# Kernel tuning notes

Hardware: AMD Instinct MI355X
Metric: run time of the kernel (lower is better)

## Reference

```python
import jax, jax.numpy as jnp
import numpy as np


def _chamfer_sq(points, gts):
    # points: [B,N,3], gts: [B,M,3]
    pn = jnp.sum(points * points, axis=-1)              # [B,N]
    gn = jnp.sum(gts * gts, axis=-1)                    # [B,M]
    cross = jnp.einsum('bnd,bmd->bnm', points, gts)     # [B,N,M]
    d = pn[:, :, None] + gn[:, None, :] - 2.0 * cross   # [B,N,M]
    d = jnp.maximum(d, 0.0)
    p2g = jnp.min(d, axis=2)                            # [B,N] squared NN dist
    g2p = jnp.min(d, axis=1)                            # [B,M]
    return p2g, g2p


def setup_inputs() -> dict:
    key = jax.random.key(0)
    k1, k2 = jax.random.split(key)
    B, N, M = 8, 4096, 4096
    points = jax.random.normal(k1, (B, N, 3), dtype=jnp.float32)
    gts = jax.random.normal(k2, (B, M, 3), dtype=jnp.float32)
    return {"points": points, "gts": gts}


def reference(points, gts):
    p2g_sq, g2p_sq = _chamfer_sq(points, gts)
    p2g = jnp.sqrt(jnp.mean(p2g_sq, axis=1))   # [B]
    g2p = jnp.sqrt(jnp.mean(g2p_sq, axis=1))   # [B]
    loss = (p2g + g2p) / 2.0
    return (jnp.mean(loss), jnp.mean(p2g), jnp.mean(g2p))
```

## Files before the change

kernel.cpp:

```cpp
#include <hip/hip_runtime.h>
#include <math.h>

#define NPTS 4096
#define NB   8
#define QCB  512
#define RCB  1024
#define NQC  (NPTS / QCB)
#define NRC  (NPTS / RCB)

typedef _Float16 h8   __attribute__((ext_vector_type(8)));
typedef float    f32x16 __attribute__((ext_vector_type(16)));

__device__ __forceinline__ void split2(float v, _Float16& h, _Float16& l) {
    h = (_Float16)v;
    l = (_Float16)(v - (float)h);
}

__global__ __launch_bounds__(1024, 1) void chamfer_mfma32(
    const float* __restrict__ P, const float* __restrict__ G,
    float* __restrict__ qpart,
    float* __restrict__ rpart)
{
    __shared__ __align__(16) unsigned char smem[77824];
    h8*   Bfr  = (h8*)smem;
    int*  rbuf = (int*)(smem + 73728);
    float* qbufall = (float*)smem;

    const int b    = blockIdx.y;
    const int qc   = blockIdx.x >> 2;
    const int rc   = blockIdx.x & 3;
    const int tid  = threadIdx.x;
    const int w    = tid >> 6;
    const int lane = tid & 63;
    const int col  = lane & 31;
    const int kg   = lane >> 5;

    const float* __restrict__ Pb = P + (size_t)b * NPTS * 3;
    const float* __restrict__ Gb = G + (size_t)b * NPTS * 3;

    const _Float16 one = (_Float16)1.f, zr = (_Float16)0.f;

    rbuf[tid] = 0x7f7fffff;
    for (int e = tid; e < 32 * 64; e += 1024) {
        const int el   = e & 63;
        const int ecol = el & 31, ekg = el >> 5;
        const int ref  = rc * RCB + (e >> 6) * 32 + ecol;
        const float gx = Gb[3 * ref], gy = Gb[3 * ref + 1], gz = Gb[3 * ref + 2];
        const float gn = fmaf(gx, gx, fmaf(gy, gy, gz * gz));
        _Float16 xh, xl, yh, yl, zh, zl, nh, nl;
        split2(gx, xh, xl); split2(gy, yh, yl); split2(gz, zh, zl); split2(gn, nh, nl);
        Bfr[e] = ekg ? (h8){one, nh, xl, yl, zl, zr, nl, zr}
                     : (h8){xh, yh, zh, one, nh, xh, yh, zh};
    }

    {
    }
    const int q0 = qc * QCB + w * 32 + col;
    const float px = Pb[3 * q0], py = Pb[3 * q0 + 1], pz = Pb[3 * q0 + 2];
    const float m2x = -2.f * px, m2y = -2.f * py, m2z = -2.f * pz;
    const float pn = fmaf(px, px, fmaf(py, py, pz * pz));
    _Float16 axh, axl, ayh, ayl, azh, azl, aph, apl;
    split2(m2x, axh, axl); split2(m2y, ayh, ayl); split2(m2z, azh, azl); split2(pn, aph, apl);
    const h8 afr = kg ? (h8){apl, zr, axh, ayh, azh, aph, one, zr}
                      : (h8){axh, ayh, azh, aph, one, axl, ayl, azl};

    f32x16 qacc;
#pragma unroll
    for (int j = 0; j < 16; ++j) qacc[j] = 3.4e38f;

    __syncthreads();

    const f32x16 cz = (f32x16){0.f,0.f,0.f,0.f,0.f,0.f,0.f,0.f,
                               0.f,0.f,0.f,0.f,0.f,0.f,0.f,0.f};
#pragma unroll 4
    for (int rt = 0; rt < 32; ++rt) {
        const h8 bfr = Bfr[rt * 64 + lane];
        f32x16 d = __builtin_amdgcn_mfma_f32_32x32x16_f16(afr, bfr, cz, 0, 0, 0);
#pragma unroll
        for (int j = 0; j < 16; ++j) qacc[j] = fminf(qacc[j], d[j]);
        float t0 = fminf(fminf(d[0],  d[1]),  d[2]);
        float t1 = fminf(fminf(d[3],  d[4]),  d[5]);
        float t2 = fminf(fminf(d[6],  d[7]),  d[8]);
        float t3 = fminf(fminf(d[9],  d[10]), d[11]);
        float t4 = fminf(fminf(d[12], d[13]), d[14]);
        float v  = fminf(fminf(fminf(t0, t1), t2), fminf(fminf(t3, t4), d[15]));
        v = fmaxf(v, 0.f);
        atomicMin(&rbuf[rt * 32 + col], __float_as_int(v));
    }

    __syncthreads();
    rpart[((size_t)b * NQC + qc) * NPTS + rc * RCB + tid] = __int_as_float(rbuf[tid]);
    __syncthreads();

    float* qw = qbufall + w * 1152;
#pragma unroll
    for (int j = 0; j < 16; ++j) {
        const int row = (j & 3) + 8 * (j >> 2) + 4 * kg;
        qw[row * 36 + col] = qacc[j];
    }
    __syncthreads();
    const float4* qr = (const float4*)(qw + col * 36);
    float4 v0 = qr[0], v1 = qr[1], v2 = qr[2], v3 = qr[3];
    float4 v4 = qr[4], v5 = qr[5], v6 = qr[6], v7 = qr[7];
    float4 m01 = make_float4(fminf(v0.x,v1.x), fminf(v0.y,v1.y), fminf(v0.z,v1.z), fminf(v0.w,v1.w));
    float4 m23 = make_float4(fminf(v2.x,v3.x), fminf(v2.y,v3.y), fminf(v2.z,v3.z), fminf(v2.w,v3.w));
    float4 m45 = make_float4(fminf(v4.x,v5.x), fminf(v4.y,v5.y), fminf(v4.z,v5.z), fminf(v4.w,v5.w));
    float4 m67 = make_float4(fminf(v6.x,v7.x), fminf(v6.y,v7.y), fminf(v6.z,v7.z), fminf(v6.w,v7.w));
    float4 ma = make_float4(fminf(m01.x,m23.x), fminf(m01.y,m23.y), fminf(m01.z,m23.z), fminf(m01.w,m23.w));
    float4 mb = make_float4(fminf(m45.x,m67.x), fminf(m45.y,m67.y), fminf(m45.z,m67.z), fminf(m45.w,m67.w));
    const float rowmin = fminf(fminf(fminf(ma.x, ma.y), fminf(ma.z, ma.w)),
                               fminf(fminf(mb.x, mb.y), fminf(mb.z, mb.w)));
    if (lane < 32)
        qpart[((size_t)b * NRC + rc) * NPTS + qc * QCB + w * 32 + col] = rowmin;
}

__global__ __launch_bounds__(256) void chamfer_reduce2(
    const float* __restrict__ qpart, const float* __restrict__ rpart,
    float* __restrict__ r16)
{
    const int path = blockIdx.x >> 3;
    const int b    = blockIdx.x & 7;
    float sum = 0.f;
    if (path == 0) {
        const float* __restrict__ base = qpart + (size_t)b * NRC * NPTS;
        for (int i = 0; i < NPTS / 256; ++i) {
            const int qq = i * 256 + threadIdx.x;
            float mn = base[qq];
#pragma unroll
            for (int c = 1; c < NRC; ++c) mn = fminf(mn, base[(size_t)c * NPTS + qq]);
            sum += fmaxf(mn, 0.f);
        }
    } else {
        const float* __restrict__ base = rpart + (size_t)b * NQC * NPTS;
        for (int i = 0; i < NPTS / 256; ++i) {
            const int qq = i * 256 + threadIdx.x;
            float mn = base[qq];
#pragma unroll
            for (int c = 1; c < NQC; ++c) mn = fminf(mn, base[(size_t)c * NPTS + qq]);
            sum += fmaxf(mn, 0.f);
        }
    }
    __shared__ float red[256];
    red[threadIdx.x] = sum;
    __syncthreads();
    if (threadIdx.x < 128) red[threadIdx.x] += red[threadIdx.x + 128];
    __syncthreads();
    if (threadIdx.x < 64) {
        float v = red[threadIdx.x] + red[threadIdx.x + 64];
#pragma unroll
        for (int off = 32; off > 0; off >>= 1) v += __shfl_down(v, off, 64);
        if (threadIdx.x == 0) r16[blockIdx.x] = sqrtf(v / (float)NPTS);
    }
}

__global__ __launch_bounds__(64) void chamfer_final(
    const float* __restrict__ r16, float* __restrict__ out)
{
    if (threadIdx.x == 0) {
        float p2g = 0.f, g2p = 0.f;
#pragma unroll
        for (int bb = 0; bb < NB; ++bb) { p2g += r16[bb]; g2p += r16[NB + bb]; }
        p2g *= (1.0f / NB);
        g2p *= (1.0f / NB);
        out[0] = 0.5f * (p2g + g2p);
        out[1] = p2g;
        out[2] = g2p;
    }
}

extern "C" void kernel_launch(void* const* d_in, const int* in_sizes, int n_in,
                              void* d_out, int out_size, void* d_ws, size_t ws_size,
                              hipStream_t stream) {
    const float* points = (const float*)d_in[0];
    const float* gts    = (const float*)d_in[1];
    float* out = (float*)d_out;

    float* qpart = (float*)d_ws;
    float* rpart = qpart + (size_t)NB * NRC * NPTS;
    float* r16   = rpart + (size_t)NB * NQC * NPTS;

    dim3 grid1(NQC * NRC, NB);
    chamfer_mfma32<<<grid1, 1024, 0, stream>>>(points, gts, qpart, rpart);

    chamfer_reduce2<<<dim3(16), 256, 0, stream>>>(qpart, rpart, r16);

    chamfer_final<<<dim3(1), 64, 0, stream>>>(r16, out);
}
```

Before: 21.00 us.

## Halve reference chunk, allow two blocks per CU, fuse final reduction via last-block counter

The reference chunk per block drops from 1024 to 512, which doubles the grid to 512 blocks. Launch bounds now allow two 1024-thread blocks per CU, and LDS is reduced to fit. The reduce kernel is split into 64 blocks, and the last block to finish, found with an atomic counter, computes the final outputs, so the separate final kernel launch goes away. In exchange there are twice as many partial rows to reduce, plus atomic and threadfence overhead. Register pressure also rises under the two-block occupancy limit.

```diff
diff --git a/kernel.cpp b/kernel.cpp
--- a/kernel.cpp
+++ b/kernel.cpp
@@ -4,11 +4,12 @@
 #define NPTS 4096
 #define NB   8
 #define QCB  512
-#define RCB  1024
+#define RCB  512
 #define NQC  (NPTS / QCB)
 #define NRC  (NPTS / RCB)
+#define NRT  (RCB / 32)
 
-typedef _Float16 h8   __attribute__((ext_vector_type(8)));
+typedef _Float16 h8     __attribute__((ext_vector_type(8)));
 typedef float    f32x16 __attribute__((ext_vector_type(16)));
 
 __device__ __forceinline__ void split2(float v, _Float16& h, _Float16& l) {
@@ -16,32 +17,35 @@
     l = (_Float16)(v - (float)h);
 }
 
-__global__ __launch_bounds__(1024, 1) void chamfer_mfma32(
+__global__ __launch_bounds__(1024, 2) void chamfer_mfma32(
     const float* __restrict__ P, const float* __restrict__ G,
     float* __restrict__ qpart,
-    float* __restrict__ rpart)
+    float* __restrict__ rpart,
+    int* __restrict__ counter)
 {
-    __shared__ __align__(16) unsigned char smem[77824];
-    h8*   Bfr  = (h8*)smem;
-    int*  rbuf = (int*)(smem + 73728);
+    __shared__ __align__(16) unsigned char smem[73728];
+    h8*    Bfr  = (h8*)smem;
+    int*   rbuf = (int*)(smem + 16384);
     float* qbufall = (float*)smem;
 
     const int b    = blockIdx.y;
-    const int qc   = blockIdx.x >> 2;
-    const int rc   = blockIdx.x & 3;
+    const int qc   = blockIdx.x >> 3;
+    const int rc   = blockIdx.x & 7;
     const int tid  = threadIdx.x;
     const int w    = tid >> 6;
     const int lane = tid & 63;
     const int col  = lane & 31;
     const int kg   = lane >> 5;
 
+    if (blockIdx.x == 0 && blockIdx.y == 0 && tid == 0) *counter = 0;
+
     const float* __restrict__ Pb = P + (size_t)b * NPTS * 3;
     const float* __restrict__ Gb = G + (size_t)b * NPTS * 3;
 
     const _Float16 one = (_Float16)1.f, zr = (_Float16)0.f;
 
-    rbuf[tid] = 0x7f7fffff;
-    for (int e = tid; e < 32 * 64; e += 1024) {
+    if (tid < 512) rbuf[tid] = 0x7f7fffff;
+    for (int e = tid; e < NRT * 64; e += 1024) {
         const int el   = e & 63;
         const int ecol = el & 31, ekg = el >> 5;
         const int ref  = rc * RCB + (e >> 6) * 32 + ecol;
@@ -53,8 +57,6 @@
                      : (h8){xh, yh, zh, one, nh, xh, yh, zh};
     }
 
-    {
-    }
     const int q0 = qc * QCB + w * 32 + col;
     const float px = Pb[3 * q0], py = Pb[3 * q0 + 1], pz = Pb[3 * q0 + 2];
     const float m2x = -2.f * px, m2y = -2.f * py, m2z = -2.f * pz;
@@ -73,7 +75,7 @@
     const f32x16 cz = (f32x16){0.f,0.f,0.f,0.f,0.f,0.f,0.f,0.f,
                                0.f,0.f,0.f,0.f,0.f,0.f,0.f,0.f};
 #pragma unroll 4
-    for (int rt = 0; rt < 32; ++rt) {
+    for (int rt = 0; rt < NRT; ++rt) {
         const h8 bfr = Bfr[rt * 64 + lane];
         f32x16 d = __builtin_amdgcn_mfma_f32_32x32x16_f16(afr, bfr, cz, 0, 0, 0);
 #pragma unroll
@@ -89,7 +91,8 @@
     }
 
     __syncthreads();
-    rpart[((size_t)b * NQC + qc) * NPTS + rc * RCB + tid] = __int_as_float(rbuf[tid]);
+    if (tid < RCB)
+        rpart[((size_t)b * NQC + qc) * NPTS + rc * RCB + tid] = __int_as_float(rbuf[tid]);
     __syncthreads();
 
     float* qw = qbufall + w * 1152;
@@ -99,48 +102,42 @@
         qw[row * 36 + col] = qacc[j];
     }
     __syncthreads();
-    const float4* qr = (const float4*)(qw + col * 36);
-    float4 v0 = qr[0], v1 = qr[1], v2 = qr[2], v3 = qr[3];
-    float4 v4 = qr[4], v5 = qr[5], v6 = qr[6], v7 = qr[7];
-    float4 m01 = make_float4(fminf(v0.x,v1.x), fminf(v0.y,v1.y), fminf(v0.z,v1.z), fminf(v0.w,v1.w));
-    float4 m23 = make_float4(fminf(v2.x,v3.x), fminf(v2.y,v3.y), fminf(v2.z,v3.z), fminf(v2.w,v3.w));
-    float4 m45 = make_float4(fminf(v4.x,v5.x), fminf(v4.y,v5.y), fminf(v4.z,v5.z), fminf(v4.w,v5.w));
-    float4 m67 = make_float4(fminf(v6.x,v7.x), fminf(v6.y,v7.y), fminf(v6.z,v7.z), fminf(v6.w,v7.w));
-    float4 ma = make_float4(fminf(m01.x,m23.x), fminf(m01.y,m23.y), fminf(m01.z,m23.z), fminf(m01.w,m23.w));
-    float4 mb = make_float4(fminf(m45.x,m67.x), fminf(m45.y,m67.y), fminf(m45.z,m67.z), fminf(m45.w,m67.w));
-    const float rowmin = fminf(fminf(fminf(ma.x, ma.y), fminf(ma.z, ma.w)),
-                               fminf(fminf(mb.x, mb.y), fminf(mb.z, mb.w)));
-    if (lane < 32)
+    if (lane < 32) {
+        const float4* qr = (const float4*)(qw + col * 36);
+        float4 v = qr[0];
+#pragma unroll
+        for (int k = 1; k < 8; ++k) {
+            float4 u = qr[k];
+            v.x = fminf(v.x, u.x); v.y = fminf(v.y, u.y);
+            v.z = fminf(v.z, u.z); v.w = fminf(v.w, u.w);
+        }
+        const float rowmin = fminf(fminf(v.x, v.y), fminf(v.z, v.w));
         qpart[((size_t)b * NRC + rc) * NPTS + qc * QCB + w * 32 + col] = rowmin;
+    }
 }
 
 __global__ __launch_bounds__(256) void chamfer_reduce2(
     const float* __restrict__ qpart, const float* __restrict__ rpart,
-    float* __restrict__ r16)
+    float* __restrict__ sums, int* __restrict__ counter,
+    float* __restrict__ out)
 {
-    const int path = blockIdx.x >> 3;
-    const int b    = blockIdx.x & 7;
+    const int path = blockIdx.x >> 5;
+    const int b    = (blockIdx.x >> 2) & 7;
+    const int sp   = blockIdx.x & 3;
+    const float* __restrict__ base = (path ? rpart : qpart) + (size_t)b * 8 * NPTS;
+
     float sum = 0.f;
-    if (path == 0) {
-        const float* __restrict__ base = qpart + (size_t)b * NRC * NPTS;
-        for (int i = 0; i < NPTS / 256; ++i) {
-            const int qq = i * 256 + threadIdx.x;
-            float mn = base[qq];
 #pragma unroll
-            for (int c = 1; c < NRC; ++c) mn = fminf(mn, base[(size_t)c * NPTS + qq]);
-            sum += fmaxf(mn, 0.f);
-        }
-    } else {
-        const float* __restrict__ base = rpart + (size_t)b * NQC * NPTS;
-        for (int i = 0; i < NPTS / 256; ++i) {
-            const int qq = i * 256 + threadIdx.x;
-            float mn = base[qq];
+    for (int i = 0; i < 4; ++i) {
+        const int q = sp * 1024 + i * 256 + threadIdx.x;
+        float mn = base[q];
 #pragma unroll
-            for (int c = 1; c < NQC; ++c) mn = fminf(mn, base[(size_t)c * NPTS + qq]);
-            sum += fmaxf(mn, 0.f);
-        }
+        for (int c = 1; c < 8; ++c) mn = fminf(mn, base[(size_t)c * NPTS + q]);
+        sum += fmaxf(mn, 0.f);
     }
+
     __shared__ float red[256];
+    __shared__ int amLast;
     red[threadIdx.x] = sum;
     __syncthreads();
     if (threadIdx.x < 128) red[threadIdx.x] += red[threadIdx.x + 128];
@@ -149,22 +146,35 @@
         float v = red[threadIdx.x] + red[threadIdx.x + 64];
 #pragma unroll
         for (int off = 32; off > 0; off >>= 1) v += __shfl_down(v, off, 64);
-        if (threadIdx.x == 0) r16[blockIdx.x] = sqrtf(v / (float)NPTS);
+        if (threadIdx.x == 0) {
+            sums[blockIdx.x] = v;
+            __threadfence();
+            amLast = (atomicAdd(counter, 1) == 63);
+        }
     }
-}
+    __syncthreads();
 
-__global__ __launch_bounds__(64) void chamfer_final(
-    const float* __restrict__ r16, float* __restrict__ out)
-{
-    if (threadIdx.x == 0) {
-        float p2g = 0.f, g2p = 0.f;
+    if (amLast) {
+        __shared__ float r16[16];
+        if (threadIdx.x < 16) {
+            float s = 0.f;
 #pragma unroll
-        for (int bb = 0; bb < NB; ++bb) { p2g += r16[bb]; g2p += r16[NB + bb]; }
-        p2g *= (1.0f / NB);
-        g2p *= (1.0f / NB);
-        out[0] = 0.5f * (p2g + g2p);
-        out[1] = p2g;
-        out[2] = g2p;
+            for (int k = 0; k < 4; ++k)
+                s += *(volatile const float*)&sums[threadIdx.x * 4 + k];
+            r16[threadIdx.x] = sqrtf(s / (float)NPTS);
+        }
+        __syncthreads();
+        if (threadIdx.x == 0) {
+            float p2g = 0.f, g2p = 0.f;
+#pragma unroll
+            for (int bb = 0; bb < NB; ++bb) { p2g += r16[bb]; g2p += r16[NB + bb]; }
+            p2g *= (1.0f / NB);
+            g2p *= (1.0f / NB);
+            out[0] = 0.5f * (p2g + g2p);
+            out[1] = p2g;
+            out[2] = g2p;
+            *counter = 0;
+        }
     }
 }
 
@@ -177,12 +187,11 @@
 
     float* qpart = (float*)d_ws;
     float* rpart = qpart + (size_t)NB * NRC * NPTS;
-    float* r16   = rpart + (size_t)NB * NQC * NPTS;
+    float* sums  = rpart + (size_t)NB * NQC * NPTS;
+    int*   counter = (int*)(sums + 64);
 
     dim3 grid1(NQC * NRC, NB);
-    chamfer_mfma32<<<grid1, 1024, 0, stream>>>(points, gts, qpart, rpart);
+    chamfer_mfma32<<<grid1, 1024, 0, stream>>>(points, gts, qpart, rpart, counter);
 
-    chamfer_reduce2<<<dim3(16), 256, 0, stream>>>(qpart, rpart, r16);
-
-    chamfer_final<<<dim3(1), 64, 0, stream>>>(r16, out);
+    chamfer_reduce2<<<dim3(64), 256, 0, stream>>>(qpart, rpart, sums, counter, out);
 }
```

Result: faster. 20.51 us (-2.3%).
